# Kernel tuning notes

Hardware: AMD Instinct MI355X
Metric: run time of the kernel (lower is better)

Reference implementation:

```python
import jax, jax.numpy as jnp
import numpy as np

NUM_ITER = 2
MIN_FILTER_REG = 1e-5
NUM_BINS = 10
BIN_DISP = 0.5
BG_MASK_VAL = 0.0
STEPLEN_REG = 0.0


def apply_filter(feat, filt):
    # feat: [1, S, C, H, W], filt: [S, NF, C, fh, fw] -> scores [1, S, NF, H, W]
    _, S, C, H, W = feat.shape
    NF, fh, fw = filt.shape[1], filt.shape[3], filt.shape[4]
    out = jax.lax.conv_general_dilated(
        feat.reshape(1, S * C, H, W),
        filt.reshape(S * NF, C, fh, fw),
        window_strides=(1, 1),
        padding=[(fh // 2, fh // 2), (fw // 2, fw // 2)],
        feature_group_count=S)
    return out.reshape(1, S, NF, H, W)


def apply_feat_transpose(feat, residuals, filt_shape):
    # gradient of apply_filter w.r.t. the filter (conv transpose on weights)
    zero = jnp.zeros(filt_shape, feat.dtype)
    _, vjp = jax.vjp(lambda w: apply_filter(feat, w), zero)
    return vjp(residuals)[0]


def distance_map(dH, dW, cy, cx):
    # pytracking DistanceMap: soft bin assignment of radial distance, [NUM_BINS, dH, dW]
    d0 = jnp.arange(dH, dtype=jnp.float32) - cy
    d1 = jnp.arange(dW, dtype=jnp.float32) - cx
    dist = jnp.sqrt(d0[:, None] ** 2 + d1[None, :] ** 2)
    bin_diff = dist[None] / BIN_DISP - jnp.arange(NUM_BINS, dtype=jnp.float32)[:, None, None]
    main = jax.nn.relu(1.0 - jnp.abs(bin_diff[:-1]))
    last = jnp.clip(1.0 + bin_diff[-1:], 0.0, 1.0)
    return jnp.concatenate([main, last], axis=0)


def unfold_map(full_map, H, W):
    # equivalent of F.unfold(...).view(H,W,H,W).flip((2,3)).permute(2,3,0,1)
    # map[i*W+j, y, x] = full_map[H-1-i+y, W-1-j+x]
    yy = (H - 1) - jnp.arange(H)[:, None] + jnp.arange(H)[None, :]  # [i, y]
    xx = (W - 1) - jnp.arange(W)[:, None] + jnp.arange(W)[None, :]  # [j, x]
    m = full_map[yy[:, None, :, None], xx[None, :, None, :]]        # [i, j, y, x]
    return m.reshape(1, 1, H * W, H, W)


def setup_inputs() -> dict:
    key = jax.random.key(0)
    k1, k2 = jax.random.split(key)
    S, C, H, W, fsz = 8, 256, 23, 23, 3
    NF = H * W
    filt = jax.random.normal(k1, (S, NF, C, fsz, fsz), jnp.float32) * 0.01
    feat = jax.random.normal(k2, (1, S, C, H, W), jnp.float32)
    # label_map_predictor init: gauss(sigma=1.0) over bin centers, min-subtracted
    d = jnp.arange(NUM_BINS, dtype=jnp.float32) * BIN_DISP
    g = jnp.exp(-0.5 * (d / 1.0) ** 2)
    w_label = g - g.min()
    w_spatial = jnp.ones((NUM_BINS,), jnp.float32)
    log_step_length = jnp.zeros((), jnp.float32)       # log(1.0)
    filter_reg = jnp.asarray(0.01, jnp.float32)
    return {"filter": filt, "feat": feat, "w_label": w_label, "w_spatial": w_spatial,
            "log_step_length": log_step_length, "filter_reg": filter_reg}


def reference(filter, feat, w_label, w_spatial, log_step_length, filter_reg):
    f = filter
    _, S, C, H, W = feat.shape
    NF = f.shape[1]
    dH, dW = 2 * H - 1, 2 * W - 1
    bins = distance_map(dH, dW, dH // 2, dW // 2)                 # [B, dH, dW]
    label_full = jnp.einsum('b,bhw->hw', w_label, bins)           # 1x1 conv
    spatial_full = jnp.einsum('b,bhw->hw', w_spatial, bins)
    label_map = unfold_map(label_full, H, W)                      # [1,1,NF,H,W]
    spatial_weight = unfold_map(spatial_full, H, W)
    tm = (1.0 - BG_MASK_VAL) * jnp.eye(NF, dtype=f.dtype).reshape(1, 1, NF, H, W) + BG_MASK_VAL
    step_length = jnp.exp(log_step_length)
    reg_weight = jnp.maximum(filter_reg * filter_reg, MIN_FILTER_REG ** 2)

    for _ in range(NUM_ITER):
        scores = apply_filter(feat, f)                            # [1,S,NF,H,W]
        # LeakyReluPar activation parameterized by target mask
        scores_act = (1.0 - tm) * 0.5 * jnp.abs(scores) + (1.0 + tm) * 0.5 * scores
        score_mask = (1.0 - tm) * 0.5 * jnp.sign(jax.lax.stop_gradient(scores)) + (1.0 + tm) * 0.5
        loss_residuals = spatial_weight * (scores_act - label_map)
        mapped_residuals = score_mask * (spatial_weight * loss_residuals)
        filter_grad = apply_feat_transpose(feat, mapped_residuals, f.shape) + reg_weight * f
        scores_grad = apply_filter(feat, filter_grad)
        scores_grad = spatial_weight * (score_mask * scores_grad)
        alpha_num = (filter_grad * filter_grad).reshape(S, NF, -1).sum(-1)   # [S, NF]
        alpha_den = jnp.maximum(
            (scores_grad * scores_grad).reshape(S, NF, -1).sum(-1) + reg_weight * alpha_num, 1e-8)
        alpha_den = alpha_den + STEPLEN_REG * alpha_num
        alpha = alpha_num / alpha_den
        f = f - step_length * alpha.reshape(S, NF, 1, 1, 1) * filter_grad
    return f
```

## Files before the change

### kernel.cpp

```cpp
#include <hip/hip_runtime.h>
#include <math.h>

#define NF   529
#define K9   2304
#define NP   544
#define DMAP 45

typedef unsigned short ush;
typedef unsigned int u32;
typedef __bf16 bf8_t __attribute__((ext_vector_type(8)));
typedef float f4_t __attribute__((ext_vector_type(4)));
typedef ush ush8 __attribute__((ext_vector_type(8)));


__device__ __forceinline__ ush f2bf(float f) {
  union { float f; u32 u; } v; v.f = f;
  u32 r = v.u + 0x7fffu + ((v.u >> 16) & 1u);
  return (ush)(r >> 16);
}
__device__ __forceinline__ float bf2f(ush h) {
  union { u32 u; float f; } v; v.u = ((u32)h) << 16;
  return v.f;
}
__device__ __forceinline__ void async16(const void* g, void* l) {
  __builtin_amdgcn_global_load_lds((const __attribute__((address_space(1))) u32*)g,
                                   (__attribute__((address_space(3))) u32*)l, 16, 0, 0);
}

__global__ void build_maps(const float* __restrict__ wl, const float* __restrict__ wsp,
                           float* __restrict__ labelF, float* __restrict__ spatialF) {
  int idx = blockIdx.x * blockDim.x + threadIdx.x;
  if (idx >= DMAP * DMAP) return;
  int h = idx / DMAP, w = idx % DMAP;
  float dy = (float)(h - 22), dx = (float)(w - 22);
  float dist = sqrtf(dy * dy + dx * dx);
  float lab = 0.f, sp = 0.f;
#pragma unroll
  for (int b = 0; b < 9; ++b) {
    float bd = dist * 2.f - (float)b;
    float wt = fmaxf(0.f, 1.f - fabsf(bd));
    lab += wl[b] * wt;
    sp  += wsp[b] * wt;
  }
  float bd = dist * 2.f - 9.f;
  float wt = fminf(fmaxf(1.f + bd, 0.f), 1.f);
  lab += wl[9] * wt;
  sp  += wsp[9] * wt;
  labelF[idx] = lab;
  spatialF[idx] = sp;
}

__global__ void convert_f(const float* __restrict__ filt, float* __restrict__ F,
                          ush* __restrict__ Fhl) {
  int g = blockIdx.x * 256 + threadIdx.x;
  int row = g / 288;
  int kk = (g - row * 288) * 8;
  int s = row / NF, m = row - s * NF;
  const float4* fp = (const float4*)(filt + (size_t)row * K9 + kk);
  float4 a = fp[0], b = fp[1];
  float4* Fp = (float4*)(F + (size_t)row * K9 + kk);
  Fp[0] = a; Fp[1] = b;
  float vv[8] = {a.x, a.y, a.z, a.w, b.x, b.y, b.z, b.w};
  ush8 h, lo;
#pragma unroll
  for (int i = 0; i < 8; ++i) {
    ush hh = f2bf(vv[i]);
    h[i] = hh;
    lo[i] = f2bf(vv[i] - bf2f(hh));
  }
  size_t o = ((size_t)s * 576 + m) * (2 * K9) + (kk >> 5) * 64 + (kk & 31);
  *(ush8*)(Fhl + o) = h;
  *(ush8*)(Fhl + o + 32) = lo;
}

__global__ void im2col_pack(const float* __restrict__ feat,
                            ush* __restrict__ Xbhl, ush* __restrict__ XThl) {
  __shared__ float T[64][65];
  int s = blockIdx.z, k0 = blockIdx.y * 64, yx0 = blockIdx.x * 64;
  int t = threadIdx.x;
  int r = t >> 2, c4 = (t & 3) * 16;
  int k = k0 + r;
  int ck = k / 9, j = k - ck * 9;
  int dy = j / 3 - 1, dx = j - (j / 3) * 3 - 1;
  const float* fb = feat + ((size_t)s * 256 + ck) * 529;
  float v[16];
#pragma unroll
  for (int i = 0; i < 16; ++i) {
    int yx = yx0 + c4 + i;
    float vv = 0.f;
    if (yx < NF) {
      int yy = yx / 23;
      int y = yy + dy, x = yx - yy * 23 + dx;
      if (y >= 0 && y < 23 && x >= 0 && x < 23) vv = fb[y * 23 + x];
    }
    v[i] = vv;
    T[r][c4 + i] = vv;
  }
  int c0 = yx0 + c4;
  if (c0 < NP) {
    size_t o = ((size_t)s * K9 + k) * (2 * NP) + (c0 >> 5) * 64 + (c0 & 31);
    ush8 h[2], lo[2];
#pragma unroll
    for (int gg = 0; gg < 2; ++gg)
#pragma unroll
      for (int i = 0; i < 8; ++i) {
        float vv = v[gg * 8 + i];
        ush hh = f2bf(vv);
        h[gg][i] = hh;
        lo[gg][i] = f2bf(vv - bf2f(hh));
      }
    *(ush8*)(Xbhl + o) = h[0];
    *(ush8*)(Xbhl + o + 8) = h[1];
    *(ush8*)(Xbhl + o + 32) = lo[0];
    *(ush8*)(Xbhl + o + 40) = lo[1];
  }
  __syncthreads();
  int kc = k0 + c4;
  size_t o2 = ((size_t)s * 640 + yx0 + r) * (2 * K9) + (kc >> 5) * 64 + (kc & 31);
  ush8 h2[2], l2[2];
#pragma unroll
  for (int gg = 0; gg < 2; ++gg)
#pragma unroll
    for (int i = 0; i < 8; ++i) {
      float vv = T[c4 + gg * 8 + i][r];
      ush hh = f2bf(vv);
      h2[gg][i] = hh;
      l2[gg][i] = f2bf(vv - bf2f(hh));
    }
  *(ush8*)(XThl + o2) = h2[0];
  *(ush8*)(XThl + o2 + 8) = h2[1];
  *(ush8*)(XThl + o2 + 32) = l2[0];
  *(ush8*)(XThl + o2 + 40) = l2[1];
}

template <int KTOT, int ASPL, int BSPL, int MODE, int SKC, int CH, int BPG, int GX>
__launch_bounds__(256, 6)
__global__ void gemm128(const ush* __restrict__ Ahl, const ush* __restrict__ Bhl,
                        float* __restrict__ Cp,
                        const float* __restrict__ F, const float* __restrict__ frp,
                        ush* __restrict__ FGhl, float* __restrict__ numb,
                        const int arows) {
  __shared__ ush As[ASPL][128 * 32];
  __shared__ ush Bs[BSPL][64 * 32];

  const int tid = threadIdx.x;
  const int w = tid >> 6, l = tid & 63;
  const int wm = w & 1, wn = w >> 1;
  const int q = l >> 4, c = l & 15;

  const int xcd = blockIdx.x & 7;
  const int t = blockIdx.x >> 3;
  const int g = xcd + 8 * (t / BPG);
  const int j = t % BPG;
  const int s = g / SKC, sk = g % SKC;
  const int x = j % GX, y = j / GX;
  const int m0 = x * 128, n0 = y * 64;

  const ush* A0 = Ahl + (size_t)s * arows * (2 * KTOT);
  const ush* B0 = Bhl + (size_t)s * ((MODE == 2) ? K9 : 640) * (2 * KTOT);

  const int srow = w * 16 + (l >> 2);
  const int scol = (l & 3) * 8;
  const int ssw  = ((((l & 3) - (l >> 3)) & 3)) * 8;
  const int rb   = tid >> 2;
  const int sb   = (tid & 3) * 8;
  const int sswb = (((tid & 3) - (tid >> 3)) & 3) * 8;

  auto stage = [&](int ch) {
    const int k2 = (sk * CH + ch) * 64;
#pragma unroll
    for (int i = 0; i < 2; ++i) {
      size_t ro = (size_t)(m0 + i * 64 + srow) * (2 * KTOT) + k2 + ssw;
      async16(A0 + ro, &As[0][(i * 64 + srow) * 32 + scol]);
      if (ASPL == 2) async16(A0 + ro + 32, &As[1][(i * 64 + srow) * 32 + scol]);
    }
    {
      size_t ro = (size_t)(n0 + rb) * (2 * KTOT) + k2 + sswb;
      async16(B0 + ro, &Bs[0][rb * 32 + sb]);
      if (BSPL == 2) async16(B0 + ro + 32, &Bs[1][rb * 32 + sb]);
    }
  };

  f4_t acc[4][2];
#pragma unroll
  for (int i = 0; i < 4; ++i)
#pragma unroll
    for (int jj = 0; jj < 2; ++jj) acc[i][jj] = (f4_t){0.f, 0.f, 0.f, 0.f};

  const int slotA = (((q + (c >> 1)) & 3)) * 8;

  stage(0);

  for (int ch = 0; ch < CH; ++ch) {
    __syncthreads();

    bf8_t av[ASPL][4], bv[BSPL][2];
#pragma unroll
    for (int pp = 0; pp < ASPL; ++pp)
#pragma unroll
      for (int ti = 0; ti < 4; ++ti)
        av[pp][ti] = *(const bf8_t*)&As[pp][(wm * 64 + ti * 16 + c) * 32 + slotA];
#pragma unroll
    for (int pp = 0; pp < BSPL; ++pp)
#pragma unroll
      for (int tj = 0; tj < 2; ++tj)
        bv[pp][tj] = *(const bf8_t*)&Bs[pp][(wn * 32 + tj * 16 + c) * 32 + slotA];

    __syncthreads();
    if (ch + 1 < CH) stage(ch + 1);

#pragma unroll
    for (int ti = 0; ti < 4; ++ti)
#pragma unroll
      for (int tj = 0; tj < 2; ++tj) {
        acc[ti][tj] = __builtin_amdgcn_mfma_f32_16x16x32_bf16(av[0][ti], bv[0][tj], acc[ti][tj], 0, 0, 0);
        if (ASPL == 2)
          acc[ti][tj] = __builtin_amdgcn_mfma_f32_16x16x32_bf16(av[1][ti], bv[0][tj], acc[ti][tj], 0, 0, 0);
        if (BSPL == 2)
          acc[ti][tj] = __builtin_amdgcn_mfma_f32_16x16x32_bf16(av[0][ti], bv[1][tj], acc[ti][tj], 0, 0, 0);
      }
  }

  if (MODE == 0) {
    float* C = Cp + (size_t)(sk * 8 + s) * 640 * 640;
#pragma unroll
    for (int ti = 0; ti < 4; ++ti)
#pragma unroll
      for (int tj = 0; tj < 2; ++tj)
#pragma unroll
        for (int r = 0; r < 4; ++r) {
          int m = m0 + wm * 64 + ti * 16 + q * 4 + r;
          int n = n0 + wn * 32 + tj * 16 + c;
          __builtin_nontemporal_store(acc[ti][tj][r], &C[(size_t)m * 640 + n]);
        }
  } else {
    float reg = fmaxf(frp[0] * frp[0], 1e-10f);
#pragma unroll
    for (int ti = 0; ti < 4; ++ti) {
      float ps[4] = {0.f, 0.f, 0.f, 0.f};
      int mb = m0 + wm * 64 + ti * 16 + q * 4;
#pragma unroll
      for (int tj = 0; tj < 2; ++tj) {
        int n = n0 + wn * 32 + tj * 16 + c;
#pragma unroll
        for (int r = 0; r < 4; ++r) {
          int m = mb + r;
          if (m < NF) {
            float v = acc[ti][tj][r] + reg * F[((size_t)s * NF + m) * K9 + n];
            size_t o = ((size_t)s * 576 + m) * (2 * K9) + ((n >> 5) * 64) + (n & 31);
            ush h = f2bf(v);
            FGhl[o] = h;
            FGhl[o + 32] = f2bf(v - bf2f(h));
            ps[r] += v * v;
          }
        }
      }
#pragma unroll
      for (int r = 0; r < 4; ++r) {
        float pp = ps[r];
        pp += __shfl_xor(pp, 1); pp += __shfl_xor(pp, 2);
        pp += __shfl_xor(pp, 4); pp += __shfl_xor(pp, 8);
        if (c == 0 && (mb + r) < NF) atomicAdd(&numb[s * NF + mb + r], pp);
      }
    }
  }
}

__global__ void reduce_epi1(const float* __restrict__ Cp,
                            const float* __restrict__ labelF, const float* __restrict__ spatialF,
                            ush* __restrict__ Rbhl, ush* __restrict__ Mb) {
  int row = blockIdx.x;
  int s = row / NF, m = row - s * NF;
  int a = m / 23, b = m - a * 23;
  const size_t sp = (size_t)8 * 640 * 640;
  const float* C = Cp + ((size_t)s * 640 + m) * 640;
  for (int n = threadIdx.x; n < NF; n += 256) {
    float v = __builtin_nontemporal_load(&C[n]) +
              __builtin_nontemporal_load(&C[sp + n]);
    int yy = n / 23, xx = n - yy * 23;
    int idx = (22 + yy - a) * DMAP + (22 + xx - b);
    float sw = spatialF[idx], lm = labelF[idx];
    float sa, msk;
    if (m == n) { sa = v; msk = 1.f; }
    else {
      sa = 0.5f * fabsf(v) + 0.5f * v;
      msk = (v > 0.f) ? 1.f : ((v < 0.f) ? 0.f : 0.5f);
    }
    float rv = msk * sw * sw * (sa - lm);
    size_t o = ((size_t)s * 640 + m) * (2 * NP) + ((n >> 5) * 64) + (n & 31);
    ush h = f2bf(rv);
    Rbhl[o] = h;
    Rbhl[o + 32] = f2bf(rv - bf2f(h));
    Mb[((size_t)s * NF + m) * NP + n] = f2bf(msk);
  }
}

__global__ void reduce_epi3(const float* __restrict__ Cp,
                            const float* __restrict__ spatialF, const ush* __restrict__ Mb,
                            float* __restrict__ denb) {
  int row = blockIdx.x;
  int s = row / NF, m = row - s * NF;
  int a = m / 23, b = m - a * 23;
  const size_t sp = (size_t)8 * 640 * 640;
  const float* C = Cp + ((size_t)s * 640 + m) * 640;
  float ss = 0.f;
  for (int n = threadIdx.x; n < NF; n += 256) {
    float v = __builtin_nontemporal_load(&C[n]) +
              __builtin_nontemporal_load(&C[sp + n]);
    int yy = n / 23, xx = n - yy * 23;
    int idx = (22 + yy - a) * DMAP + (22 + xx - b);
    float sw = spatialF[idx];
    float msk = bf2f(Mb[((size_t)s * NF + m) * NP + n]);
    float z = sw * msk * v;
    ss += z * z;
  }
  __shared__ float red[256];
  red[threadIdx.x] = ss; __syncthreads();
  for (int st = 128; st > 0; st >>= 1) {
    if (threadIdx.x < st) red[threadIdx.x] += red[threadIdx.x + st];
    __syncthreads();
  }
  if (threadIdx.x == 0) denb[row] = red[0];
}

__global__ void update_f(float* __restrict__ F, const ush* __restrict__ FGhl,
                         const float* __restrict__ numb, const float* __restrict__ denb,
                         const float* __restrict__ lsp, const float* __restrict__ frp,
                         ush* __restrict__ Fhl) {
  int g = blockIdx.x * 256 + threadIdx.x;
  int row = g / 288;
  int kk = (g - row * 288) * 8;
  int s = row / NF, m = row - s * NF;
  float reg = fmaxf(frp[0] * frp[0], 1e-10f);
  float nm = numb[row], dn = denb[row];
  float alpha = nm / fmaxf(dn + reg * nm, 1e-8f);
  float sa = expf(lsp[0]) * alpha;
  size_t o = ((size_t)s * 576 + m) * (2 * K9) + (kk >> 5) * 64 + (kk & 31);
  ush8 gh = *(const ush8*)(FGhl + o);
  ush8 gl = *(const ush8*)(FGhl + o + 32);
  float4* Fp = (float4*)(F + (size_t)row * K9 + kk);
  float4 a = Fp[0], b = Fp[1];
  float f[8] = {a.x, a.y, a.z, a.w, b.x, b.y, b.z, b.w};
  ush8 h, lo;
#pragma unroll
  for (int i = 0; i < 8; ++i) {
    f[i] -= sa * (bf2f(gh[i]) + bf2f(gl[i]));
    ush hh = f2bf(f[i]);
    h[i] = hh;
    lo[i] = f2bf(f[i] - bf2f(hh));
  }
  Fp[0] = (float4){f[0], f[1], f[2], f[3]};
  Fp[1] = (float4){f[4], f[5], f[6], f[7]};
  *(ush8*)(Fhl + o) = h;
  *(ush8*)(Fhl + o + 32) = lo;
}

extern "C" void kernel_launch(void* const* d_in, const int* in_sizes, int n_in,
                              void* d_out, int out_size, void* d_ws, size_t ws_size,
                              hipStream_t stream) {
  const float* filt = (const float*)d_in[0];
  const float* feat = (const float*)d_in[1];
  const float* wl   = (const float*)d_in[2];
  const float* wsp  = (const float*)d_in[3];
  const float* lsp  = (const float*)d_in[4];
  const float* frp  = (const float*)d_in[5];
  float* F = (float*)d_out;

  float* fb       = (float*)d_ws;
  float* labelF   = fb;
  float* spatialF = fb + 2048;
  float* numden   = fb + 4096;
  ush* cur = (ush*)(fb + 4096 + 4 * 4240);

  const size_t szF  = (size_t)8 * 576 * (2 * K9);
  const size_t szXT = (size_t)8 * 640 * (2 * K9);
  const size_t szXb = (size_t)8 * K9 * (2 * NP);
  const size_t szRb = (size_t)8 * 640 * (2 * NP);
  const size_t szMb = (size_t)8 * NF * NP;

  ush* Fhl  = cur;           cur += szF;
  ush* FGhl = cur;           cur += szF;
  ush* XThl = cur;           cur += szXT;
  ush* Xbhl = cur;           cur += szXb;
  ush* Rbhl = cur;           cur += szRb;
  ush* Mb   = cur;           cur += szMb;
  float* Cp = (float*)((((size_t)cur) + 15) & ~(size_t)15);

  build_maps<<<8, 256, 0, stream>>>(wl, wsp, labelF, spatialF);
  hipMemsetAsync(numden, 0, 4 * 4240 * sizeof(float), stream);
  convert_f<<<4761, 256, 0, stream>>>(filt, F, Fhl);
  im2col_pack<<<dim3(10, 36, 8), 256, 0, stream>>>(feat, Xbhl, XThl);

  for (int it = 0; it < 2; ++it) {
    float* numb = numden + it * 2 * 4240;
    float* denb = numb + 4240;
    gemm128<K9, 2, 2, 0, 2, 36, 45, 5><<<720, 256, 0, stream>>>(
        Fhl, XThl, Cp, nullptr, nullptr, nullptr, nullptr, 576);
    reduce_epi1<<<8 * NF, 256, 0, stream>>>(Cp, labelF, spatialF, Rbhl, Mb);
    gemm128<NP, 2, 2, 2, 1, 17, 180, 5><<<1440, 256, 0, stream>>>(
        Rbhl, Xbhl, nullptr, F, frp, FGhl, numb, 640);
    gemm128<K9, 1, 1, 0, 2, 36, 45, 5><<<720, 256, 0, stream>>>(
        FGhl, XThl, Cp, nullptr, nullptr, nullptr, nullptr, 576);
    reduce_epi3<<<8 * NF, 256, 0, stream>>>(Cp, spatialF, Mb, denb);
    update_f<<<4761, 256, 0, stream>>>(F, FGhl, numb, denb, lsp, frp, Fhl);
  }
}
```

Baseline: 497.4 us.

## Derive second-iteration scores by linearity and skip idle warps on tail tiles

Filter application is linear, so the second iteration's scores are computed as S - step*alpha*G from the saved first-iteration scores and scores_grad. This drops one forward GEMM over K=2304. The first-iteration scores_grad GEMM now uses the full-precision hi/lo split so the reconstructed scores stay accurate. The GEMM kernel also skips loads, MFMAs and stores for the wave rows of the last M tile that fall past the valid rows. The cost is extra fp32 scores and gradient buffers written and read back.

Measured after the change: 780.3 us. 56.9% more time.

```diff
diff --git a/kernel.cpp b/kernel.cpp
--- a/kernel.cpp
+++ b/kernel.cpp
@@ -156,6 +156,9 @@
   const int x = j % GX, y = j / GX;
   const int m0 = x * 128, n0 = y * 64;
 
+  const bool tail = (x == GX - 1);
+  const bool wact = (!tail) || (wm == 0);
+
   const ush* A0 = Ahl + (size_t)s * arows * (2 * KTOT);
   const ush* B0 = Bhl + (size_t)s * ((MODE == 2) ? K9 : 640) * (2 * KTOT);
 
@@ -170,6 +173,7 @@
     const int k2 = (sk * CH + ch) * 64;
 #pragma unroll
     for (int i = 0; i < 2; ++i) {
+      if (i == 1 && tail) break;
       size_t ro = (size_t)(m0 + i * 64 + srow) * (2 * KTOT) + k2 + ssw;
       async16(A0 + ro, &As[0][(i * 64 + srow) * 32 + scol]);
       if (ASPL == 2) async16(A0 + ro + 32, &As[1][(i * 64 + srow) * 32 + scol]);
@@ -195,45 +199,51 @@
     __syncthreads();
 
     bf8_t av[ASPL][4], bv[BSPL][2];
-#pragma unroll
-    for (int pp = 0; pp < ASPL; ++pp)
-#pragma unroll
-      for (int ti = 0; ti < 4; ++ti)
-        av[pp][ti] = *(const bf8_t*)&As[pp][(wm * 64 + ti * 16 + c) * 32 + slotA];
-#pragma unroll
-    for (int pp = 0; pp < BSPL; ++pp)
-#pragma unroll
-      for (int tj = 0; tj < 2; ++tj)
-        bv[pp][tj] = *(const bf8_t*)&Bs[pp][(wn * 32 + tj * 16 + c) * 32 + slotA];
+    if (wact) {
+#pragma unroll
+      for (int pp = 0; pp < ASPL; ++pp)
+#pragma unroll
+        for (int ti = 0; ti < 4; ++ti)
+          av[pp][ti] = *(const bf8_t*)&As[pp][(wm * 64 + ti * 16 + c) * 32 + slotA];
+#pragma unroll
+      for (int pp = 0; pp < BSPL; ++pp)
+#pragma unroll
+        for (int tj = 0; tj < 2; ++tj)
+          bv[pp][tj] = *(const bf8_t*)&Bs[pp][(wn * 32 + tj * 16 + c) * 32 + slotA];
+    }
 
     __syncthreads();
     if (ch + 1 < CH) stage(ch + 1);
 
-#pragma unroll
-    for (int ti = 0; ti < 4; ++ti)
-#pragma unroll
-      for (int tj = 0; tj < 2; ++tj) {
-        acc[ti][tj] = __builtin_amdgcn_mfma_f32_16x16x32_bf16(av[0][ti], bv[0][tj], acc[ti][tj], 0, 0, 0);
-        if (ASPL == 2)
-          acc[ti][tj] = __builtin_amdgcn_mfma_f32_16x16x32_bf16(av[1][ti], bv[0][tj], acc[ti][tj], 0, 0, 0);
-        if (BSPL == 2)
-          acc[ti][tj] = __builtin_amdgcn_mfma_f32_16x16x32_bf16(av[0][ti], bv[1][tj], acc[ti][tj], 0, 0, 0);
-      }
+    if (wact) {
+#pragma unroll
+      for (int ti = 0; ti < 4; ++ti)
+#pragma unroll
+        for (int tj = 0; tj < 2; ++tj) {
+          acc[ti][tj] = __builtin_amdgcn_mfma_f32_16x16x32_bf16(av[0][ti], bv[0][tj], acc[ti][tj], 0, 0, 0);
+          if (ASPL == 2)
+            acc[ti][tj] = __builtin_amdgcn_mfma_f32_16x16x32_bf16(av[1][ti], bv[0][tj], acc[ti][tj], 0, 0, 0);
+          if (BSPL == 2)
+            acc[ti][tj] = __builtin_amdgcn_mfma_f32_16x16x32_bf16(av[0][ti], bv[1][tj], acc[ti][tj], 0, 0, 0);
+        }
+    }
   }
 
   if (MODE == 0) {
-    float* C = Cp + (size_t)(sk * 8 + s) * 640 * 640;
-#pragma unroll
-    for (int ti = 0; ti < 4; ++ti)
-#pragma unroll
-      for (int tj = 0; tj < 2; ++tj)
-#pragma unroll
-        for (int r = 0; r < 4; ++r) {
-          int m = m0 + wm * 64 + ti * 16 + q * 4 + r;
-          int n = n0 + wn * 32 + tj * 16 + c;
-          __builtin_nontemporal_store(acc[ti][tj][r], &C[(size_t)m * 640 + n]);
-        }
-  } else {
+    if (wact) {
+      float* C = Cp + (size_t)(sk * 8 + s) * 640 * 640;
+#pragma unroll
+      for (int ti = 0; ti < 4; ++ti)
+#pragma unroll
+        for (int tj = 0; tj < 2; ++tj)
+#pragma unroll
+          for (int r = 0; r < 4; ++r) {
+            int m = m0 + wm * 64 + ti * 16 + q * 4 + r;
+            int n = n0 + wn * 32 + tj * 16 + c;
+            __builtin_nontemporal_store(acc[ti][tj][r], &C[(size_t)m * 640 + n]);
+          }
+    }
+  } else if (wact) {
     float reg = fmaxf(frp[0] * frp[0], 1e-10f);
 #pragma unroll
     for (int ti = 0; ti < 4; ++ti) {
@@ -268,7 +278,8 @@
 
 __global__ void reduce_epi1(const float* __restrict__ Cp,
                             const float* __restrict__ labelF, const float* __restrict__ spatialF,
-                            ush* __restrict__ Rbhl, ush* __restrict__ Mb) {
+                            ush* __restrict__ Rbhl, ush* __restrict__ Mb,
+                            float* __restrict__ Sv) {
   int row = blockIdx.x;
   int s = row / NF, m = row - s * NF;
   int a = m / 23, b = m - a * 23;
@@ -277,6 +288,7 @@
   for (int n = threadIdx.x; n < NF; n += 256) {
     float v = __builtin_nontemporal_load(&C[n]) +
               __builtin_nontemporal_load(&C[sp + n]);
+    Sv[(size_t)row * 544 + n] = v;
     int yy = n / 23, xx = n - yy * 23;
     int idx = (22 + yy - a) * DMAP + (22 + xx - b);
     float sw = spatialF[idx], lm = labelF[idx];
@@ -297,7 +309,7 @@
 
 __global__ void reduce_epi3(const float* __restrict__ Cp,
                             const float* __restrict__ spatialF, const ush* __restrict__ Mb,
-                            float* __restrict__ denb) {
+                            float* __restrict__ denb, float* __restrict__ Gv) {
   int row = blockIdx.x;
   int s = row / NF, m = row - s * NF;
   int a = m / 23, b = m - a * 23;
@@ -307,6 +319,7 @@
   for (int n = threadIdx.x; n < NF; n += 256) {
     float v = __builtin_nontemporal_load(&C[n]) +
               __builtin_nontemporal_load(&C[sp + n]);
+    if (Gv) Gv[(size_t)row * 544 + n] = v;
     int yy = n / 23, xx = n - yy * 23;
     int idx = (22 + yy - a) * DMAP + (22 + xx - b);
     float sw = spatialF[idx];
@@ -321,6 +334,40 @@
     __syncthreads();
   }
   if (threadIdx.x == 0) denb[row] = red[0];
+}
+
+__global__ void scores2_fused(const float* __restrict__ Sv, const float* __restrict__ Gv,
+                              const float* __restrict__ numb, const float* __restrict__ denb,
+                              const float* __restrict__ lsp, const float* __restrict__ frp,
+                              const float* __restrict__ labelF, const float* __restrict__ spatialF,
+                              ush* __restrict__ Rbhl, ush* __restrict__ Mb) {
+  int row = blockIdx.x;
+  int s = row / NF, m = row - s * NF;
+  int a = m / 23, b = m - a * 23;
+  float reg = fmaxf(frp[0] * frp[0], 1e-10f);
+  float nm = numb[row], dn = denb[row];
+  float alpha = nm / fmaxf(dn + reg * nm, 1e-8f);
+  float sa2 = expf(lsp[0]) * alpha;
+  const float* S = Sv + (size_t)row * 544;
+  const float* G = Gv + (size_t)row * 544;
+  for (int n = threadIdx.x; n < NF; n += 256) {
+    float v = S[n] - sa2 * G[n];
+    int yy = n / 23, xx = n - yy * 23;
+    int idx = (22 + yy - a) * DMAP + (22 + xx - b);
+    float sw = spatialF[idx], lm = labelF[idx];
+    float sa, msk;
+    if (m == n) { sa = v; msk = 1.f; }
+    else {
+      sa = 0.5f * fabsf(v) + 0.5f * v;
+      msk = (v > 0.f) ? 1.f : ((v < 0.f) ? 0.f : 0.5f);
+    }
+    float rv = msk * sw * sw * (sa - lm);
+    size_t o = ((size_t)s * 640 + m) * (2 * NP) + ((n >> 5) * 64) + (n & 31);
+    ush h = f2bf(rv);
+    Rbhl[o] = h;
+    Rbhl[o + 32] = f2bf(rv - bf2f(h));
+    Mb[((size_t)s * NF + m) * NP + n] = f2bf(msk);
+  }
 }
 
 __global__ void update_f(float* __restrict__ F, const ush* __restrict__ FGhl,
@@ -377,6 +424,7 @@
   const size_t szXb = (size_t)8 * K9 * (2 * NP);
   const size_t szRb = (size_t)8 * 640 * (2 * NP);
   const size_t szMb = (size_t)8 * NF * NP;
+  const size_t szSv = (size_t)8 * NF * 544;
 
   ush* Fhl  = cur;           cur += szF;
   ush* FGhl = cur;           cur += szF;
@@ -384,6 +432,8 @@
   ush* Xbhl = cur;           cur += szXb;
   ush* Rbhl = cur;           cur += szRb;
   ush* Mb   = cur;           cur += szMb;
+  float* Sb = (float*)cur;   cur += szSv * 2;
+  float* Gb = (float*)cur;   cur += szSv * 2;
   float* Cp = (float*)((((size_t)cur) + 15) & ~(size_t)15);
 
   build_maps<<<8, 256, 0, stream>>>(wl, wsp, labelF, spatialF);
@@ -391,17 +441,27 @@
   convert_f<<<4761, 256, 0, stream>>>(filt, F, Fhl);
   im2col_pack<<<dim3(10, 36, 8), 256, 0, stream>>>(feat, Xbhl, XThl);
 
-  for (int it = 0; it < 2; ++it) {
-    float* numb = numden + it * 2 * 4240;
-    float* denb = numb + 4240;
-    gemm128<K9, 2, 2, 0, 2, 36, 45, 5><<<720, 256, 0, stream>>>(
-        Fhl, XThl, Cp, nullptr, nullptr, nullptr, nullptr, 576);
-    reduce_epi1<<<8 * NF, 256, 0, stream>>>(Cp, labelF, spatialF, Rbhl, Mb);
-    gemm128<NP, 2, 2, 2, 1, 17, 180, 5><<<1440, 256, 0, stream>>>(
-        Rbhl, Xbhl, nullptr, F, frp, FGhl, numb, 640);
-    gemm128<K9, 1, 1, 0, 2, 36, 45, 5><<<720, 256, 0, stream>>>(
-        FGhl, XThl, Cp, nullptr, nullptr, nullptr, nullptr, 576);
-    reduce_epi3<<<8 * NF, 256, 0, stream>>>(Cp, spatialF, Mb, denb);
-    update_f<<<4761, 256, 0, stream>>>(F, FGhl, numb, denb, lsp, frp, Fhl);
-  }
-}
+  float* numb0 = numden;
+  float* denb0 = numden + 4240;
+  float* numb1 = numden + 2 * 4240;
+  float* denb1 = numden + 3 * 4240;
+
+  gemm128<K9, 2, 2, 0, 2, 36, 45, 5><<<720, 256, 0, stream>>>(
+      Fhl, XThl, Cp, nullptr, nullptr, nullptr, nullptr, 576);
+  reduce_epi1<<<8 * NF, 256, 0, stream>>>(Cp, labelF, spatialF, Rbhl, Mb, Sb);
+  gemm128<NP, 2, 2, 2, 1, 17, 180, 5><<<1440, 256, 0, stream>>>(
+      Rbhl, Xbhl, nullptr, F, frp, FGhl, numb0, 640);
+  gemm128<K9, 2, 2, 0, 2, 36, 45, 5><<<720, 256, 0, stream>>>(
+      FGhl, XThl, Cp, nullptr, nullptr, nullptr, nullptr, 576);
+  reduce_epi3<<<8 * NF, 256, 0, stream>>>(Cp, spatialF, Mb, denb0, Gb);
+  update_f<<<4761, 256, 0, stream>>>(F, FGhl, numb0, denb0, lsp, frp, Fhl);
+
+  scores2_fused<<<8 * NF, 256, 0, stream>>>(Sb, Gb, numb0, denb0, lsp, frp,
+                                            labelF, spatialF, Rbhl, Mb);
+  gemm128<NP, 2, 2, 2, 1, 17, 180, 5><<<1440, 256, 0, stream>>>(
+      Rbhl, Xbhl, nullptr, F, frp, FGhl, numb1, 640);
+  gemm128<K9, 1, 1, 0, 2, 36, 45, 5><<<720, 256, 0, stream>>>(
+      FGhl, XThl, Cp, nullptr, nullptr, nullptr, nullptr, 576);
+  reduce_epi3<<<8 * NF, 256, 0, stream>>>(Cp, spatialF, Mb, denb1, nullptr);
+  update_f<<<4761, 256, 0, stream>>>(F, FGhl, numb1, denb1, lsp, frp, Fhl);
+}
```
